# Performance work log

Measured on AMD Instinct MI355X. Metric: run time of the kernel, lower is better.

The kernel has to match this reference:

```python
import jax, jax.numpy as jnp
import numpy as np

E, K, H, I = 8, 2, 768, 1152  # experts, top_k, hidden, intermediate
T = 4096  # total tokens


def setup_inputs() -> dict:
    key = jax.random.key(0)
    ks = jax.random.split(key, 6)
    return {
        "x": jax.random.normal(ks[0], (T, H), jnp.float32),
        "gate_w": jax.random.normal(ks[1], (E, H), jnp.float32) * 0.02,
        "correction_bias": jnp.zeros((E,), jnp.float32),
        "Wi": jax.random.normal(ks[2], (E, H, 2 * I), jnp.float32) * 0.02,
        "Wo": jax.random.normal(ks[3], (E, I, H), jnp.float32) * 0.02,
        "shared_Wi": jax.random.normal(ks[4], (2 * I, H), jnp.float32) * 0.02,
        "shared_Wo": jax.random.normal(ks[5], (H, I), jnp.float32) * 0.02,
    }


def reference(x, gate_w, correction_bias, Wi, Wo, shared_Wi, shared_Wo):
    # ---- shared SwiGLU expert (dropout=0 in eval) ----
    sh = x @ shared_Wi.T                      # (T, 2I)
    s_in, s_gate = sh[:, :I], sh[:, I:]
    shared_out = (jax.nn.silu(s_in) * s_gate) @ shared_Wo.T  # (T, H)

    # ---- sigmoid top-k router with bias correction ----
    logits = jax.nn.sigmoid(x @ gate_w.T)     # (T, E)
    sel = logits + correction_bias
    _, indices = jax.lax.top_k(sel, K)        # (T, K)
    weights = jnp.take_along_axis(logits, indices, axis=-1)  # bias-free scores
    weights = weights / jnp.sum(weights, axis=-1, keepdims=True)

    # combine weight per (expert, token): cw[e, t] = sum_k weights[t,k]*[indices[t,k]==e]
    one_hot = jax.nn.one_hot(indices, E, dtype=x.dtype)      # (T, K, E)
    cw = jnp.einsum("tke,tk->et", one_hot, weights)          # (E, T)

    # ---- experts: SwiGLU per expert, weighted scatter-combine ----
    h = jnp.einsum("th,ehf->etf", x, Wi)      # (E, T, 2I)
    proj, gate = h[..., :I], h[..., I:]
    act = jax.nn.silu(gate) * proj            # (E, T, I)
    act = act * cw[:, :, None]                # fold combine weights before Wo
    expert_out = jnp.einsum("eti,eih->th", act, Wo)          # (T, H)

    return expert_out + shared_out
```

## Files before the change

### kernel.cpp

```cpp
#include <hip/hip_runtime.h>
#include <stdint.h>

#define E_  8
#define H_  768
#define I_  1152
#define T_  4096
#define F2_ (2*I_)

typedef unsigned short u16;
typedef __attribute__((ext_vector_type(8))) __bf16 bf16x8;
typedef __attribute__((ext_vector_type(4))) float floatx4;

typedef const void __attribute__((address_space(1))) as1_void;
typedef void __attribute__((address_space(3))) as3_void;

__device__ __forceinline__ void gld16(void* lds, const void* g) {
  __builtin_amdgcn_global_load_lds((as1_void*)g, (as3_void*)lds, 16, 0, 0);
}

__device__ __forceinline__ u16 f2bf(float f) {
  union { float f; unsigned int i; } v; v.f = f;
  unsigned int r = v.i + 0x7FFF + ((v.i >> 16) & 1);
  return (u16)(r >> 16);
}

__device__ __forceinline__ void transpose_core(u16 (*tile)[68],
                                               const float* __restrict__ src,
                                               u16* __restrict__ dst,
                                               int R, int C, int xi, int yi, int zi) {
  const float* s = src + (long)zi * R * C;
  u16*         d = dst + (long)zi * R * C;
  int r0 = yi * 64, c0 = xi * 64;
  int c4 = (threadIdx.x & 15) * 4;
  int rr = threadIdx.x >> 4;
  #pragma unroll
  for (int k = 0; k < 64; k += 16) {
    float4 v = *(const float4*)(s + (long)(r0 + rr + k) * C + (c0 + c4));
    ushort4 u;
    u.x = f2bf(v.x); u.y = f2bf(v.y); u.z = f2bf(v.z); u.w = f2bf(v.w);
    *(ushort4*)&tile[rr + k][c4] = u;
  }
  __syncthreads();
  int c  = threadIdx.x >> 2;
  int rq = (threadIdx.x & 3) * 4;
  #pragma unroll
  for (int k = 0; k < 64; k += 16) {
    ushort4 u;
    u.x = tile[rq + k + 0][c];
    u.y = tile[rq + k + 1][c];
    u.z = tile[rq + k + 2][c];
    u.w = tile[rq + k + 3][c];
    *(ushort4*)(d + (long)(c0 + c) * R + (r0 + rq + k)) = u;
  }
}

#define GATE_BLKS (T_ / 4)
#define CONV_BLKS ((F2_ * H_ + H_ * I_) / 1024)
#define TWI_X (F2_ / 64)
#define TWI_Y (H_ / 64)
#define TWI_BLKS (TWI_X * TWI_Y * E_)
#define TWO_X (H_ / 64)
#define TWO_Y (I_ / 64)
#define TWO_BLKS (TWO_X * TWO_Y * E_)
#define PREP_BLKS (GATE_BLKS + CONV_BLKS + TWI_BLKS)

__global__ __launch_bounds__(256)
void prep_all(const float* __restrict__ x, const float* __restrict__ gw,
              const float* __restrict__ bias,
              int* __restrict__ top2e, float* __restrict__ top2w, u16* __restrict__ xb,
              const float* __restrict__ sWi, u16* __restrict__ sWib,
              const float* __restrict__ sWo, u16* __restrict__ sWob,
              const float* __restrict__ Wi, u16* __restrict__ WiT) {
  __shared__ u16 tile[64][68];
  int b = blockIdx.x;
  if (b < GATE_BLKS) {
    int t    = b * 4 + (threadIdx.x >> 6);
    int lane = threadIdx.x & 63;
    float acc[E_];
    #pragma unroll
    for (int e = 0; e < E_; e++) acc[e] = 0.f;
    #pragma unroll
    for (int i = 0; i < H_ / 256; i++) {
      int c = i * 256 + lane * 4;
      float4 xv = *(const float4*)(x + (long)t * H_ + c);
      ushort4 u;
      u.x = f2bf(xv.x); u.y = f2bf(xv.y); u.z = f2bf(xv.z); u.w = f2bf(xv.w);
      *(ushort4*)(xb + (long)t * H_ + c) = u;
      #pragma unroll
      for (int e = 0; e < E_; e++) {
        float4 g = *(const float4*)(gw + e * H_ + c);
        acc[e] += xv.x * g.x + xv.y * g.y + xv.z * g.z + xv.w * g.w;
      }
    }
    #pragma unroll
    for (int e = 0; e < E_; e++) {
      #pragma unroll
      for (int s = 32; s > 0; s >>= 1) acc[e] += __shfl_xor(acc[e], s);
    }
    if (lane == 0) {
      float logits[E_], sel[E_];
      #pragma unroll
      for (int e = 0; e < E_; e++) {
        logits[e] = 1.f / (1.f + expf(-acc[e]));
        sel[e]    = logits[e] + bias[e];
      }
      int i0 = 0;
      #pragma unroll
      for (int e = 1; e < E_; e++) if (sel[e] > sel[i0]) i0 = e;
      int i1 = (i0 == 0) ? 1 : 0;
      #pragma unroll
      for (int e = 0; e < E_; e++) if (e != i0 && sel[e] > sel[i1]) i1 = e;
      float w0 = logits[i0], w1 = logits[i1], s = w0 + w1;
      top2e[t * 2 + 0] = i0;  top2w[t * 2 + 0] = w0 / s;
      top2e[t * 2 + 1] = i1;  top2w[t * 2 + 1] = w1 / s;
    }
  } else if (b < GATE_BLKS + CONV_BLKS) {
    int i = ((b - GATE_BLKS) * 256 + threadIdx.x) * 4;
    const int n1 = F2_ * H_;
    const float* s; u16* d;
    if (i < n1) { s = sWi + i; d = sWib + i; }
    else        { s = sWo + (i - n1); d = sWob + (i - n1); }
    float4 v = *(const float4*)s;
    ushort4 u;
    u.x = f2bf(v.x); u.y = f2bf(v.y); u.z = f2bf(v.z); u.w = f2bf(v.w);
    *(ushort4*)d = u;
  } else {
    int i = b - (GATE_BLKS + CONV_BLKS);
    int xi = i % TWI_X, yi = (i / TWI_X) % TWI_Y, zi = i / (TWI_X * TWI_Y);
    transpose_core(tile, Wi, WiT, H_, F2_, xi, yi, zi);
  }
}

__global__ void build_lists(const int* __restrict__ top2e, const float* __restrict__ top2w,
                            int* __restrict__ counts, int* __restrict__ offs,
                            int* __restrict__ list, float* __restrict__ wlist,
                            int* __restrict__ pos) {
  __shared__ int scnt[4][E_];
  __shared__ int sq[4];
  __shared__ int soffs[E_];
  int e = blockIdx.x;
  int tid = threadIdx.x, w = tid >> 6, lane = tid & 63;
  const int Q = (2 * T_) / 4;

  int c8[E_];
  #pragma unroll
  for (int q = 0; q < E_; q++) c8[q] = 0;
  for (int i = tid; i < 2 * T_; i += 256) {
    int v = top2e[i];
    #pragma unroll
    for (int q = 0; q < E_; q++) c8[q] += (v == q);
  }
  int qstart = w * Q;
  int ce = 0;
  for (int i = qstart + lane; i < qstart + Q; i += 64) ce += (top2e[i] == e);
  #pragma unroll
  for (int q = 0; q < E_; q++)
    #pragma unroll
    for (int s = 32; s > 0; s >>= 1) c8[q] += __shfl_xor(c8[q], s);
  #pragma unroll
  for (int s = 32; s > 0; s >>= 1) ce += __shfl_xor(ce, s);
  if (lane == 0) {
    #pragma unroll
    for (int q = 0; q < E_; q++) scnt[w][q] = c8[q];
    sq[w] = ce;
  }
  __syncthreads();
  if (tid == 0) {
    int s = 0;
    #pragma unroll
    for (int q = 0; q < E_; q++) {
      int tot = scnt[0][q] + scnt[1][q] + scnt[2][q] + scnt[3][q];
      soffs[q] = s;
      if (e == 0) { counts[q] = tot; offs[q] = s; }
      s += tot;
    }
    if (e == 0) { counts[8] = T_; offs[8] = 2 * T_; }
  }
  __syncthreads();
  int base = soffs[e];
  #pragma unroll
  for (int w2 = 0; w2 < 4; w2++) if (w2 < w) base += sq[w2];
  unsigned long long lt = (lane == 63) ? (~0ull >> 1) : ((1ull << lane) - 1);
  for (int i0 = qstart; i0 < qstart + Q; i0 += 64) {
    int s = i0 + lane;
    bool m = (top2e[s] == e);
    unsigned long long mask = __ballot(m);
    if (m) {
      int p = base + __popcll(mask & lt);
      list[p]  = s >> 1;
      wlist[p] = top2w[s];
      pos[s]   = p;
    }
    base += __popcll(mask);
  }
  for (int t = e * (T_ / 8) + tid; t < (e + 1) * (T_ / 8); t += 256) {
    list[2 * T_ + t]  = t;
    wlist[2 * T_ + t] = 1.f;
  }
}

#define PP1 168
#define G1_BLKS (32 * PP1)
__global__ __launch_bounds__(256, 2)
void gemm_act_all(const u16* __restrict__ A, const u16* __restrict__ WiT,
                  const u16* __restrict__ sWib, u16* __restrict__ act,
                  const int* __restrict__ list, const float* __restrict__ wlist,
                  const int* __restrict__ counts, const int* __restrict__ offsets,
                  const float* __restrict__ Wo, u16* __restrict__ WoT) {
  __shared__ __align__(16) u16 As[128 * 64];
  __shared__ __align__(16) u16 Bs[2][64 * 64];

  int id = blockIdx.x;
  if (id >= G1_BLKS) {
    int i = id - G1_BLKS;
    int xi = i % TWO_X, yi = (i / TWO_X) % TWO_Y, zi = i / (TWO_X * TWO_Y);
    transpose_core((u16(*)[68])As, Wo, WoT, I_, H_, xi, yi, zi);
    return;
  }
  int y  = id / PP1, p = id - y * PP1;
  if (p >= 162) return;
  int z = p / 18, xblk = p - z * 18;

  int cnt = counts[z], off = offsets[z];
  int row0 = y * 128;
  if (row0 >= cnt) return;
  const u16* B = (z == 8) ? sWib : (WiT + (long)z * F2_ * H_);
  int n0 = xblk * 64;

  int tid  = threadIdx.x;
  int lane = tid & 63, wv = tid >> 6;
  int wr   = wv >> 1, wc = wv & 1;
  int half = lane & 15, quad = lane >> 4;

  int rA  = tid >> 3;
  int lc8 = ((tid & 7) ^ (rA & 7)) * 8;
  const u16* ap[4];
  #pragma unroll
  for (int n = 0; n < 4; n++) {
    int rr = min(row0 + rA + n * 32, cnt - 1);
    ap[n] = A + (long)list[off + rr] * H_ + lc8;
  }
  const u16* bp[2][2];
  #pragma unroll
  for (int h = 0; h < 2; h++)
    #pragma unroll
    for (int m = 0; m < 2; m++)
      bp[h][m] = B + (long)(h * I_ + n0 + m * 32 + rA) * H_ + lc8;

  floatx4 acc[2][4][2];
  #pragma unroll
  for (int q = 0; q < 2; q++)
    #pragma unroll
    for (int i = 0; i < 4; i++)
      #pragma unroll
      for (int j = 0; j < 2; j++) acc[q][i][j] = (floatx4)0.f;

  for (int k0 = 0; k0 < H_; k0 += 64) {
    if (k0) __syncthreads();
    #pragma unroll
    for (int n = 0; n < 4; n++) gld16(As + (n * 256 + tid) * 8, ap[n] + k0);
    #pragma unroll
    for (int h = 0; h < 2; h++)
      #pragma unroll
      for (int m = 0; m < 2; m++) gld16(Bs[h] + (m * 256 + tid) * 8, bp[h][m] + k0);
    __syncthreads();
    #pragma unroll
    for (int kk = 0; kk < 2; kk++) {
      int cs = ((kk * 4 + quad) ^ (half & 7)) * 8;
      bf16x8 a[4], bq[2][2];
      #pragma unroll
      for (int i = 0; i < 4; i++)
        a[i] = *(const bf16x8*)(As + (wr * 64 + i * 16 + half) * 64 + cs);
      #pragma unroll
      for (int q = 0; q < 2; q++)
        #pragma unroll
        for (int j = 0; j < 2; j++)
          bq[q][j] = *(const bf16x8*)(Bs[q] + (wc * 32 + j * 16 + half) * 64 + cs);
      #pragma unroll
      for (int i = 0; i < 4; i++)
        #pragma unroll
        for (int q = 0; q < 2; q++)
          #pragma unroll
          for (int j = 0; j < 2; j++)
            acc[q][i][j] = __builtin_amdgcn_mfma_f32_16x16x32_bf16(a[i], bq[q][j], acc[q][i][j], 0, 0, 0);
    }
  }

  bool sh = (z == 8);
  #pragma unroll
  for (int i = 0; i < 4; i++) {
    #pragma unroll
    for (int r = 0; r < 4; r++) {
      int g = row0 + wr * 64 + i * 16 + quad * 4 + r;
      if (g < cnt) {
        float w = wlist[off + g];
        #pragma unroll
        for (int j = 0; j < 2; j++) {
          float va = acc[0][i][j][r];
          float vb = acc[1][i][j][r];
          float zz = sh ? va : vb;
          float o  = sh ? vb : va;
          float sg = zz / (1.f + expf(-zz));
          float v  = sg * o * w;
          int col  = n0 + wc * 32 + j * 16 + half;
          act[(long)(off + g) * I_ + col] = f2bf(v);
        }
      }
    }
  }
}

#define PP2 40
__global__ __launch_bounds__(256, 4)
void gemm_out_all(const u16* __restrict__ A, const u16* __restrict__ WoT,
                  const u16* __restrict__ sWob, float* __restrict__ out,
                  float* __restrict__ eobuf,
                  const int* __restrict__ counts, const int* __restrict__ offsets) {
  __shared__ __align__(16) u16 As[64 * 64];
  __shared__ __align__(16) u16 Bs[192 * 64];

  int id = blockIdx.x;
  int y  = id / PP2, p = id - y * PP2;
  if (p >= 36) return;
  int z = p / 4, xblk = p - z * 4;

  int cnt = counts[z], off = offsets[z];
  int row0 = y * 64;
  if (row0 >= cnt) return;
  const u16* B = (z == 8) ? sWob : (WoT + (long)z * H_ * I_);
  int n0 = xblk * 192;

  int tid  = threadIdx.x;
  int lane = tid & 63, wv = tid >> 6;
  int wr   = wv >> 1, wc = wv & 1;
  int half = lane & 15, quad = lane >> 4;

  int rA  = tid >> 3;
  int lc8 = ((tid & 7) ^ (rA & 7)) * 8;
  const u16* ap[2];
  #pragma unroll
  for (int n = 0; n < 2; n++) {
    long rr = off + min(row0 + rA + n * 32, cnt - 1);
    ap[n] = A + rr * I_ + lc8;
  }
  const u16* bp[6];
  #pragma unroll
  for (int m = 0; m < 6; m++)
    bp[m] = B + (long)(n0 + m * 32 + rA) * I_ + lc8;

  floatx4 acc[2][6];
  #pragma unroll
  for (int i = 0; i < 2; i++)
    #pragma unroll
    for (int j = 0; j < 6; j++) acc[i][j] = (floatx4)0.f;

  for (int k0 = 0; k0 < I_; k0 += 64) {
    if (k0) __syncthreads();
    #pragma unroll
    for (int n = 0; n < 2; n++) gld16(As + (n * 256 + tid) * 8, ap[n] + k0);
    #pragma unroll
    for (int m = 0; m < 6; m++) gld16(Bs + (m * 256 + tid) * 8, bp[m] + k0);
    __syncthreads();
    #pragma unroll
    for (int kk = 0; kk < 2; kk++) {
      int cs = ((kk * 4 + quad) ^ (half & 7)) * 8;
      bf16x8 a[2], b[6];
      #pragma unroll
      for (int i = 0; i < 2; i++)
        a[i] = *(const bf16x8*)(As + (wr * 32 + i * 16 + half) * 64 + cs);
      #pragma unroll
      for (int j = 0; j < 6; j++)
        b[j] = *(const bf16x8*)(Bs + (wc * 96 + j * 16 + half) * 64 + cs);
      #pragma unroll
      for (int i = 0; i < 2; i++)
        #pragma unroll
        for (int j = 0; j < 6; j++)
          acc[i][j] = __builtin_amdgcn_mfma_f32_16x16x32_bf16(a[i], b[j], acc[i][j], 0, 0, 0);
    }
  }

  bool sh = (z == 8);
  #pragma unroll
  for (int i = 0; i < 2; i++) {
    #pragma unroll
    for (int r = 0; r < 4; r++) {
      int g = row0 + wr * 32 + i * 16 + quad * 4 + r;
      if (g < cnt) {
        float* orow = sh ? (out + (long)g * H_) : (eobuf + (long)(off + g) * H_);
        #pragma unroll
        for (int j = 0; j < 6; j++) {
          int col = n0 + wc * 96 + j * 16 + half;
          orow[col] = acc[i][j][r];
        }
      }
    }
  }
}

__global__ void final_reduce(float* __restrict__ out, const float* __restrict__ eobuf,
                             const int* __restrict__ pos) {
  int gid = blockIdx.x * 256 + threadIdx.x;
  int t = gid / (H_ / 4), c = (gid % (H_ / 4)) * 4;
  int p0 = pos[t * 2], p1 = pos[t * 2 + 1];
  float4 a = *(const float4*)(out   + (long)t  * H_ + c);
  float4 b = *(const float4*)(eobuf + (long)p0 * H_ + c);
  float4 d = *(const float4*)(eobuf + (long)p1 * H_ + c);
  a.x += b.x + d.x; a.y += b.y + d.y; a.z += b.z + d.z; a.w += b.w + d.w;
  *(float4*)(out + (long)t * H_ + c) = a;
}

extern "C" void kernel_launch(void* const* d_in, const int* in_sizes, int n_in,
                              void* d_out, int out_size, void* d_ws, size_t ws_size,
                              hipStream_t stream) {
  const float* x      = (const float*)d_in[0];
  const float* gate_w = (const float*)d_in[1];
  const float* bias   = (const float*)d_in[2];
  const float* Wi     = (const float*)d_in[3];
  const float* Wo     = (const float*)d_in[4];
  const float* sWi    = (const float*)d_in[5];
  const float* sWo    = (const float*)d_in[6];
  float* out          = (float*)d_out;

  char* ws = (char*)d_ws;
  size_t o = 0;
  auto alloc = [&](size_t bytes) -> void* {
    o = (o + 255) & ~(size_t)255;
    void* p = ws + o;
    o += bytes;
    return p;
  };
  u16*   xb    = (u16*)  alloc((size_t)T_ * H_ * 2);
  u16*   sWib  = (u16*)  alloc((size_t)F2_ * H_ * 2);
  u16*   sWob  = (u16*)  alloc((size_t)H_ * I_ * 2);
  u16*   WiT   = (u16*)  alloc((size_t)E_ * F2_ * H_ * 2);
  u16*   WoT   = (u16*)  alloc((size_t)E_ * H_ * I_ * 2);
  u16*   act   = (u16*)  alloc((size_t)3 * T_ * I_ * 2);
  int*   top2e = (int*)  alloc((size_t)T_ * 2 * 4);
  float* top2w = (float*)alloc((size_t)T_ * 2 * 4);
  int*   count = (int*)  alloc(9 * 4);
  int*   offs  = (int*)  alloc(9 * 4);
  int*   list  = (int*)  alloc((size_t)3 * T_ * 4);
  float* wlist = (float*)alloc((size_t)3 * T_ * 4);
  int*   pos   = (int*)  alloc((size_t)2 * T_ * 4);
  float* eobuf = (float*)WiT;

  prep_all<<<PREP_BLKS, 256, 0, stream>>>(x, gate_w, bias, top2e, top2w, xb,
                                          sWi, sWib, sWo, sWob, Wi, WiT);
  build_lists<<<E_, 256, 0, stream>>>(top2e, top2w, count, offs, list, wlist, pos);

  gemm_act_all<<<G1_BLKS + TWO_BLKS, 256, 0, stream>>>(xb, WiT, sWib, act, list, wlist,
                                                       count, offs, Wo, WoT);
  gemm_out_all<<<64 * PP2, 256, 0, stream>>>(act, WoT, sWob, out, eobuf, count, offs);
  final_reduce<<<(T_ * (H_ / 4)) / 256, 256, 0, stream>>>(out, eobuf, pos);
}
```

Before: 291.7 us.

## Double-buffer LDS tiles in expert up-projection GEMM to overlap loads with MFMA

Splits the shared-memory A/B tiles into two buffers and restructures the K loop so the next 64-wide K slice is fetched via global_load_lds while the current one is computed. Explicit vmcnt/lgkmcnt waits with sched barriers replace __syncthreads. This hides global load latency but doubles LDS use to 64 KB per block, which may reduce occupancy below the two blocks per CU requested by the launch bounds.

```diff
diff --git a/kernel.cpp b/kernel.cpp
--- a/kernel.cpp
+++ b/kernel.cpp
@@ -23,6 +23,13 @@
   unsigned int r = v.i + 0x7FFF + ((v.i >> 16) & 1);
   return (u16)(r >> 16);
 }
+
+#define VM_WAIT(N)  asm volatile("s_waitcnt vmcnt(" #N ")" ::: "memory")
+#define LGKM_WAIT0  asm volatile("s_waitcnt lgkmcnt(0)" ::: "memory")
+#define SFENCE()    __builtin_amdgcn_sched_barrier(0)
+#define SBAR()      __builtin_amdgcn_s_barrier()
+#define SYNC_VM(N)  do { VM_WAIT(N); SFENCE(); SBAR(); SFENCE(); } while (0)
+#define SYNC_LGKM() do { LGKM_WAIT0; SFENCE(); SBAR(); SFENCE(); } while (0)
 
 __device__ __forceinline__ void transpose_core(u16 (*tile)[68],
                                                const float* __restrict__ src,
@@ -207,14 +214,16 @@
                   const int* __restrict__ list, const float* __restrict__ wlist,
                   const int* __restrict__ counts, const int* __restrict__ offsets,
                   const float* __restrict__ Wo, u16* __restrict__ WoT) {
-  __shared__ __align__(16) u16 As[128 * 64];
-  __shared__ __align__(16) u16 Bs[2][64 * 64];
+  __shared__ __align__(16) u16 As0[128 * 64];
+  __shared__ __align__(16) u16 As1[128 * 64];
+  __shared__ __align__(16) u16 Bs0[2 * 64 * 64];
+  __shared__ __align__(16) u16 Bs1[2 * 64 * 64];
 
   int id = blockIdx.x;
   if (id >= G1_BLKS) {
     int i = id - G1_BLKS;
     int xi = i % TWO_X, yi = (i / TWO_X) % TWO_Y, zi = i / (TWO_X * TWO_Y);
-    transpose_core((u16(*)[68])As, Wo, WoT, I_, H_, xi, yi, zi);
+    transpose_core((u16(*)[68])As0, Wo, WoT, I_, H_, xi, yi, zi);
     return;
   }
   int y  = id / PP1, p = id - y * PP1;
@@ -255,27 +264,28 @@
       #pragma unroll
       for (int j = 0; j < 2; j++) acc[q][i][j] = (floatx4)0.f;
 
-  for (int k0 = 0; k0 < H_; k0 += 64) {
-    if (k0) __syncthreads();
-    #pragma unroll
-    for (int n = 0; n < 4; n++) gld16(As + (n * 256 + tid) * 8, ap[n] + k0);
-    #pragma unroll
-    for (int h = 0; h < 2; h++)
-      #pragma unroll
-      for (int m = 0; m < 2; m++) gld16(Bs[h] + (m * 256 + tid) * 8, bp[h][m] + k0);
-    __syncthreads();
+  auto stage = [&](u16* as, u16* bs, int k0) {
+    #pragma unroll
+    for (int n = 0; n < 4; n++) gld16(as + (n * 256 + tid) * 8, ap[n] + k0);
+    #pragma unroll
+    for (int h2 = 0; h2 < 2; h2++)
+      #pragma unroll
+      for (int m = 0; m < 2; m++)
+        gld16(bs + h2 * 4096 + (m * 256 + tid) * 8, bp[h2][m] + k0);
+  };
+  auto compute = [&](const u16* as, const u16* bs) {
     #pragma unroll
     for (int kk = 0; kk < 2; kk++) {
       int cs = ((kk * 4 + quad) ^ (half & 7)) * 8;
       bf16x8 a[4], bq[2][2];
       #pragma unroll
       for (int i = 0; i < 4; i++)
-        a[i] = *(const bf16x8*)(As + (wr * 64 + i * 16 + half) * 64 + cs);
+        a[i] = *(const bf16x8*)(as + (wr * 64 + i * 16 + half) * 64 + cs);
       #pragma unroll
       for (int q = 0; q < 2; q++)
         #pragma unroll
         for (int j = 0; j < 2; j++)
-          bq[q][j] = *(const bf16x8*)(Bs[q] + (wc * 32 + j * 16 + half) * 64 + cs);
+          bq[q][j] = *(const bf16x8*)(bs + q * 4096 + (wc * 32 + j * 16 + half) * 64 + cs);
       #pragma unroll
       for (int i = 0; i < 4; i++)
         #pragma unroll
@@ -284,7 +294,24 @@
           for (int j = 0; j < 2; j++)
             acc[q][i][j] = __builtin_amdgcn_mfma_f32_16x16x32_bf16(a[i], bq[q][j], acc[q][i][j], 0, 0, 0);
     }
-  }
+  };
+
+  stage(As0, Bs0, 0);
+  for (int k0 = 0; k0 < H_ - 128; k0 += 128) {
+    stage(As1, Bs1, k0 + 64);
+    SYNC_VM(8);
+    compute(As0, Bs0);
+    SYNC_LGKM();
+    stage(As0, Bs0, k0 + 128);
+    SYNC_VM(8);
+    compute(As1, Bs1);
+    SYNC_LGKM();
+  }
+  stage(As1, Bs1, H_ - 64);
+  SYNC_VM(8);
+  compute(As0, Bs0);
+  SYNC_VM(0);
+  compute(As1, Bs1);
 
   bool sh = (z == 8);
   #pragma unroll
```

Measured after the change: 296.8 us. About the same (+1.8%).
